# Kernel tuning notes

Measured on AMD Instinct MI355X. Metric: run time of the kernel, lower is better.

Reference implementation:

```python
import jax, jax.numpy as jnp
import numpy as np

NX = 2048
NY = 2048
DX = 0.01
DY = 0.01


def setup_inputs() -> dict:
    key = jax.random.key(0)
    ks = jax.random.split(key, 6)
    u = jax.random.normal(ks[0], (NX, NY), dtype=jnp.float32)
    # per-point MLP: Linear(1->32) tanh Linear(32->32) tanh Linear(32->1), no bias
    W1 = jax.random.normal(ks[1], (1, 32), dtype=jnp.float32) * 0.5
    W2 = jax.random.normal(ks[2], (32, 32), dtype=jnp.float32) * (1.0 / jnp.sqrt(32.0))
    W3 = jax.random.normal(ks[3], (32, 1), dtype=jnp.float32) * (1.0 / jnp.sqrt(32.0))
    D = jnp.array([0.01], dtype=jnp.float32)          # diffusion coeff, num_vars=1
    BC = jnp.array([[1.0], [0.0]], dtype=jnp.float32)  # [num_bound=2, num_vars=1]
    stencil = jnp.array([-1.0, 1.0], dtype=jnp.float32)
    return {"u": u, "W1": W1, "W2": W2, "W3": W3, "D": D, "BC": BC, "stencil": stencil}


def _flux_kernel(u, W1, W2, W3, D, BC, stencil):
    # func_nn applied pointwise: u[...,None] -> [Nx,Ny,1]
    h = jnp.tanh(u[..., None] @ W1)      # [Nx,Ny,32]
    h = jnp.tanh(h @ W2)                 # [Nx,Ny,32]
    a = (h @ W3)[..., 0]                 # [Nx,Ny]

    a_plus = jax.nn.relu(a)
    a_min = -jax.nn.relu(-a)

    s0, s1 = stencil[0], stencil[1]
    bc0, bc1 = BC[0, 0], BC[1, 0]
    d = D[0]

    # shifted-neighbor fields with BC values filling the boundary row/col
    u_left = jnp.concatenate([jnp.full((1, NY), bc0, u.dtype), u[:-1, :]], axis=0)
    u_right = jnp.concatenate([u[1:, :], jnp.full((1, NY), bc1, u.dtype)], axis=0)
    u_bot = jnp.concatenate([jnp.full((NX, 1), bc0, u.dtype), u[:, :-1]], axis=1)
    u_top = jnp.concatenate([u[:, 1:], jnp.full((NX, 1), bc1, u.dtype)], axis=1)

    left_flux = d * (s0 * u + s1 * u_left) - a_plus / DX * (-s0 * u - s1 * u_left)
    right_flux = d * (s0 * u + s1 * u_right) - a_min / DX * (s0 * u + s1 * u_right)
    bottom_flux = d * (s0 * u + s1 * u_bot) - a_plus / DY * (-s0 * u - s1 * u_bot)
    top_flux = d * (s0 * u + s1 * u_top) - a_min / DY * (s0 * u + s1 * u_top)

    return left_flux + right_flux + bottom_flux + top_flux


def reference(u, W1, W2, W3, D, BC, stencil):
    # state_kernel(t, u) == flux_kernel(t, u); this is du/dt at one ODE step
    return _flux_kernel(u, W1, W2, W3, D, BC, stencil)
```

## Files before the change

### kernel.cpp

```cpp
#include <hip/hip_runtime.h>

#define NXg 2048
#define NYg 2048
#define TAB_N 4096
#define TAB_LO   -8.0f
#define TAB_SCALE 256.0f
#define INV_DX 100.0f
#define INV_DY 100.0f

__global__ void build_table(const float* __restrict__ W1,
                            const float* __restrict__ W2,
                            const float* __restrict__ W3,
                            float* __restrict__ tab) {
    const int lane   = threadIdx.x & 63;
    const int half   = lane >> 5;
    const int j      = lane & 31;
    const int waveid = (blockIdx.x * blockDim.x + threadIdx.x) >> 6;
    const int node   = waveid * 2 + half;
    const int node_c = node <= TAB_N ? node : TAB_N;

    const float x = TAB_LO + (float)node_c * (1.0f / TAB_SCALE);
    const float t = tanhf(x * W1[j]);

    float z = 0.0f;
    #pragma unroll
    for (int k = 0; k < 32; ++k) {
        const float h1k = __shfl(t, (half << 5) | k);
        z = fmaf(h1k, W2[k * 32 + j], z);
    }
    float v = tanhf(z) * W3[j];
    #pragma unroll
    for (int m = 1; m < 32; m <<= 1) v += __shfl_xor(v, m);

    if (j == 0 && node <= TAB_N) tab[node] = v;
}

__launch_bounds__(1024)
__global__ void flux_kernel(const float* __restrict__ u,
                            const float* __restrict__ tab,
                            const float* __restrict__ Dp,
                            const float* __restrict__ BCp,
                            const float* __restrict__ St,
                            float* __restrict__ out) {
    __shared__ float stab[TAB_N + 1];
    for (int t = threadIdx.x; t <= TAB_N; t += blockDim.x) stab[t] = tab[t];
    __syncthreads();

    const float d   = Dp[0];
    const float bc0 = BCp[0];
    const float bc1 = BCp[1];
    const float s0  = St[0];
    const float s1  = St[1];

    const int gid  = blockIdx.x * blockDim.x + threadIdx.x;
    const int base = gid << 2;
    const int i    = base >> 11;
    const int j    = base & (NYg - 1);

    const float4 c = *reinterpret_cast<const float4*>(u + base);
    float4 L, R;
    if (i > 0)        L = *reinterpret_cast<const float4*>(u + base - NYg);
    else              L = make_float4(bc0, bc0, bc0, bc0);
    if (i < NXg - 1)  R = *reinterpret_cast<const float4*>(u + base + NYg);
    else              R = make_float4(bc1, bc1, bc1, bc1);
    const float um1 = (j > 0)       ? u[base - 1] : bc0;
    const float up4 = (j + 4 < NYg) ? u[base + 4] : bc1;

    const float uc[4] = {c.x, c.y, c.z, c.w};
    const float ul[4] = {L.x, L.y, L.z, L.w};
    const float ur[4] = {R.x, R.y, R.z, R.w};
    const float ub[4] = {um1, c.x, c.y, c.z};
    const float ut[4] = {c.y, c.z, c.w, up4};

    float res[4];
    #pragma unroll
    for (int e = 0; e < 4; ++e) {
        float t = (uc[e] - TAB_LO) * TAB_SCALE;
        t = fminf(fmaxf(t, 0.0f), 4095.999f);
        int   i0 = (int)t;
        float fr = t - (float)i0;
        float a0 = stab[i0];
        float a  = fmaf(fr, stab[i0 + 1] - a0, a0);

        const float ap = fmaxf(a, 0.0f);
        const float am = fminf(a, 0.0f);

        const float gl = s0 * uc[e] + s1 * ul[e];
        const float gr = s0 * uc[e] + s1 * ur[e];
        const float gb = s0 * uc[e] + s1 * ub[e];
        const float gt = s0 * uc[e] + s1 * ut[e];

        res[e] = (d + ap * INV_DX) * gl + (d - am * INV_DX) * gr
               + (d + ap * INV_DY) * gb + (d - am * INV_DY) * gt;
    }
    *reinterpret_cast<float4*>(out + base) = make_float4(res[0], res[1], res[2], res[3]);
}

extern "C" void kernel_launch(void* const* d_in, const int* in_sizes, int n_in,
                              void* d_out, int out_size, void* d_ws, size_t ws_size,
                              hipStream_t stream) {
    const float* u  = (const float*)d_in[0];
    const float* W1 = (const float*)d_in[1];
    const float* W2 = (const float*)d_in[2];
    const float* W3 = (const float*)d_in[3];
    const float* D  = (const float*)d_in[4];
    const float* BC = (const float*)d_in[5];
    const float* St = (const float*)d_in[6];
    float* out = (float*)d_out;
    float* tab = (float*)d_ws;

    hipLaunchKernelGGL(build_table, dim3((TAB_N / 8) + 1), dim3(256), 0, stream,
                       W1, W2, W3, tab);

    const int n_threads = (NXg * NYg) / 4;
    hipLaunchKernelGGL(flux_kernel, dim3(n_threads / 1024), dim3(1024), 0, stream,
                       u, tab, D, BC, St, out);
}
```

Before: 89.01 us.

## Process eight points per thread and store value-slope pairs in shared table

Each thread now handles eight contiguous points instead of four, halving the grid size. That also halves how often each block reloads the shared lookup table. The table is stored as (value, delta) float2 pairs, so each lookup is one LDS read plus an fma instead of two reads. The flux arithmetic is regrouped algebraically using DX equal to DY to cut multiplies. In exchange, per-thread register use goes up and fewer blocks are in flight to hide memory latency.

```diff
diff --git a/kernel.cpp b/kernel.cpp
--- a/kernel.cpp
+++ b/kernel.cpp
@@ -5,8 +5,7 @@
 #define TAB_N 4096
 #define TAB_LO   -8.0f
 #define TAB_SCALE 256.0f
-#define INV_DX 100.0f
-#define INV_DY 100.0f
+#define INV_D 100.0f
 
 __global__ void build_table(const float* __restrict__ W1,
                             const float* __restrict__ W2,
@@ -42,58 +41,74 @@
                             const float* __restrict__ BCp,
                             const float* __restrict__ St,
                             float* __restrict__ out) {
-    __shared__ float stab[TAB_N + 1];
-    for (int t = threadIdx.x; t <= TAB_N; t += blockDim.x) stab[t] = tab[t];
+    __shared__ float2 stab[TAB_N];
+    for (int t = threadIdx.x; t < TAB_N; t += 1024) {
+        const float a0 = tab[t];
+        const float a1 = tab[t + 1];
+        stab[t] = make_float2(a0, a1 - a0);
+    }
     __syncthreads();
 
-    const float d   = Dp[0];
-    const float bc0 = BCp[0];
-    const float bc1 = BCp[1];
-    const float s0  = St[0];
-    const float s1  = St[1];
+    const float d      = Dp[0];
+    const float bc0    = BCp[0];
+    const float bc1    = BCp[1];
+    const float s0     = St[0];
+    const float s1     = St[1];
+    const float two_s0 = s0 + s0;
 
     const int gid  = blockIdx.x * blockDim.x + threadIdx.x;
-    const int base = gid << 2;
+    const int base = gid << 3;
     const int i    = base >> 11;
     const int j    = base & (NYg - 1);
 
-    const float4 c = *reinterpret_cast<const float4*>(u + base);
-    float4 L, R;
-    if (i > 0)        L = *reinterpret_cast<const float4*>(u + base - NYg);
-    else              L = make_float4(bc0, bc0, bc0, bc0);
-    if (i < NXg - 1)  R = *reinterpret_cast<const float4*>(u + base + NYg);
-    else              R = make_float4(bc1, bc1, bc1, bc1);
-    const float um1 = (j > 0)       ? u[base - 1] : bc0;
-    const float up4 = (j + 4 < NYg) ? u[base + 4] : bc1;
+    const float4 c0 = *reinterpret_cast<const float4*>(u + base);
+    const float4 c1 = *reinterpret_cast<const float4*>(u + base + 4);
+    float4 L0, L1, R0, R1;
+    if (i > 0) {
+        L0 = *reinterpret_cast<const float4*>(u + base - NYg);
+        L1 = *reinterpret_cast<const float4*>(u + base - NYg + 4);
+    } else {
+        L0 = L1 = make_float4(bc0, bc0, bc0, bc0);
+    }
+    if (i < NXg - 1) {
+        R0 = *reinterpret_cast<const float4*>(u + base + NYg);
+        R1 = *reinterpret_cast<const float4*>(u + base + NYg + 4);
+    } else {
+        R0 = R1 = make_float4(bc1, bc1, bc1, bc1);
+    }
+    const float um1 = (j > 0)           ? u[base - 1] : bc0;
+    const float up8 = (j + 8 < NYg)     ? u[base + 8] : bc1;
 
-    const float uc[4] = {c.x, c.y, c.z, c.w};
-    const float ul[4] = {L.x, L.y, L.z, L.w};
-    const float ur[4] = {R.x, R.y, R.z, R.w};
-    const float ub[4] = {um1, c.x, c.y, c.z};
-    const float ut[4] = {c.y, c.z, c.w, up4};
+    const float uc[8] = {c0.x, c0.y, c0.z, c0.w, c1.x, c1.y, c1.z, c1.w};
+    const float ul[8] = {L0.x, L0.y, L0.z, L0.w, L1.x, L1.y, L1.z, L1.w};
+    const float ur[8] = {R0.x, R0.y, R0.z, R0.w, R1.x, R1.y, R1.z, R1.w};
+    const float ub[8] = {um1,  c0.x, c0.y, c0.z, c0.w, c1.x, c1.y, c1.z};
+    const float ut[8] = {c0.y, c0.z, c0.w, c1.x, c1.y, c1.z, c1.w, up8};
 
-    float res[4];
+    float res[8];
     #pragma unroll
-    for (int e = 0; e < 4; ++e) {
-        float t = (uc[e] - TAB_LO) * TAB_SCALE;
+    for (int e = 0; e < 8; ++e) {
+        float t = fmaf(uc[e], TAB_SCALE, 2048.0f);
         t = fminf(fmaxf(t, 0.0f), 4095.999f);
-        int   i0 = (int)t;
-        float fr = t - (float)i0;
-        float a0 = stab[i0];
-        float a  = fmaf(fr, stab[i0 + 1] - a0, a0);
+        const int   i0 = (int)t;
+        const float fr = t - (float)i0;
+        const float2 p = stab[i0];
+        const float a  = fmaf(fr, p.y, p.x);
 
         const float ap = fmaxf(a, 0.0f);
         const float am = fminf(a, 0.0f);
+        const float cp = fmaf(ap,  INV_D, d);
+        const float cm = fmaf(am, -INV_D, d);
 
-        const float gl = s0 * uc[e] + s1 * ul[e];
-        const float gr = s0 * uc[e] + s1 * ur[e];
-        const float gb = s0 * uc[e] + s1 * ub[e];
-        const float gt = s0 * uc[e] + s1 * ut[e];
-
-        res[e] = (d + ap * INV_DX) * gl + (d - am * INV_DX) * gr
-               + (d + ap * INV_DY) * gb + (d - am * INV_DY) * gt;
+        const float g2 = two_s0 * uc[e];
+        const float gp = fmaf(s1, ul[e] + ub[e], g2);
+        const float gm = fmaf(s1, ur[e] + ut[e], g2);
+        res[e] = fmaf(cm, gm, cp * gp);
     }
-    *reinterpret_cast<float4*>(out + base) = make_float4(res[0], res[1], res[2], res[3]);
+    float4 o0 = make_float4(res[0], res[1], res[2], res[3]);
+    float4 o1 = make_float4(res[4], res[5], res[6], res[7]);
+    *reinterpret_cast<float4*>(out + base)     = o0;
+    *reinterpret_cast<float4*>(out + base + 4) = o1;
 }
 
 extern "C" void kernel_launch(void* const* d_in, const int* in_sizes, int n_in,
@@ -112,7 +127,7 @@
     hipLaunchKernelGGL(build_table, dim3((TAB_N / 8) + 1), dim3(256), 0, stream,
                        W1, W2, W3, tab);
 
-    const int n_threads = (NXg * NYg) / 4;
+    const int n_threads = (NXg * NYg) / 8;
     hipLaunchKernelGGL(flux_kernel, dim3(n_threads / 1024), dim3(1024), 0, stream,
                        u, tab, D, BC, St, out);
 }
```

After: 86.99 us. 1.02x faster.
